# Kernel tuning notes

Measured on AMD Instinct MI355X. Metric: run time of the kernel, lower is better.

Reference implementation:

```python
import jax, jax.numpy as jnp
import numpy as np

NEG_INF = -2.0**32 + 1.0  # matches torch paddings value


def prelu(x, a):
    return jnp.where(x >= 0, x, a * x)


def setup_inputs() -> dict:
    key = jax.random.key(0)
    ks = jax.random.split(key, 12)
    B, L, D, A = 2048, 200, 128, 64
    return {
        "query": jax.random.normal(ks[0], (B, D), jnp.float32),
        "keys": jax.random.normal(ks[1], (B, L, D), jnp.float32),
        "keys_length": jax.random.randint(ks[2], (B,), 0, L, jnp.int64 if jax.config.jax_enable_x64 else jnp.int32),
        "W1": jax.random.normal(ks[3], (4 * D, A), jnp.float32) * (1.0 / np.sqrt(4 * D)),
        "b1": jax.random.normal(ks[4], (A,), jnp.float32) * 0.01,
        "a1": jnp.full((1,), 0.25, jnp.float32),  # PReLU default init
        "W2": jax.random.normal(ks[5], (A, A), jnp.float32) * (1.0 / np.sqrt(A)),
        "b2": jax.random.normal(ks[6], (A,), jnp.float32) * 0.01,
        "a2": jnp.full((1,), 0.25, jnp.float32),
        "W3": jax.random.normal(ks[7], (A, 1), jnp.float32) * (1.0 / np.sqrt(A)),
        "b3": jax.random.normal(ks[8], (1,), jnp.float32) * 0.01,
    }


def reference(query, keys, keys_length, W1, b1, a1, W2, b2, a2, W3, b3):
    B, L, D = keys.shape
    q = jnp.broadcast_to(query[:, None, :], (B, L, D))
    # concat features: [q, k, q-k, q*k] -> (B, L, 4D)
    q_k = jnp.concatenate([q, keys, q - keys, q * keys], axis=-1)
    h = prelu(jnp.einsum("blf,fa->bla", q_k, W1) + b1, a1)
    h = prelu(jnp.einsum("bla,ac->blc", h, W2) + b2, a2)
    scores = (jnp.einsum("bla,ao->blo", h, W3) + b3)[..., 0]  # (B, L)
    mask = jnp.arange(L)[None, :] < keys_length[:, None]
    scores = jnp.where(mask, scores, NEG_INF)
    att = jax.nn.softmax(scores, axis=1)
    out = jnp.einsum("bl,bld->bd", att, keys)  # bmm(att[:,None,:], keys)
    return out, att
```

## Files before the change

kernel.cpp:

```cpp
#include <hip/hip_runtime.h>
#include <math.h>

typedef __attribute__((ext_vector_type(8))) _Float16 half8;
typedef __attribute__((ext_vector_type(4))) float float4_t;

#define NB 2048
#define LL 200
#define DD 128
#define AA 64
#define NEG_INF_F -4294967295.0f

#define WQ_STRIDE 136
#define W2_STRIDE 72
#define H1_STRIDE 72

__global__ __launch_bounds__(256, 4)
void din_fused(const float* __restrict__ query,
               const float* __restrict__ keys,
               const int*   __restrict__ keys_length,
               const float* __restrict__ W1,
               const float* __restrict__ b1,
               const float* __restrict__ a1p,
               const float* __restrict__ W2,
               const float* __restrict__ b2,
               const float* __restrict__ a2p,
               const float* __restrict__ W3,
               float* __restrict__ out,
               float* __restrict__ att)
{
    __shared__ __align__(16) _Float16 sWqT[AA * WQ_STRIDE];
    __shared__ __align__(16) _Float16 sW2T[AA * W2_STRIDE];
    __shared__ __align__(16) _Float16 sH1[4 * 16 * H1_STRIDE];
    __shared__ float sQ[DD];
    __shared__ float sQW[AA];
    __shared__ float sS[224];
    __shared__ float sRed[256];

    const int tid  = threadIdx.x;
    const int b    = blockIdx.x;
    const int len  = keys_length[b];
    const float pa1 = a1p[0], pa2 = a2p[0];
    const int lane = tid & 63, wv = tid >> 6;
    const int col  = lane & 15, quad = lane >> 4;

    if (tid < DD) sQ[tid] = query[(size_t)b * DD + tid];
    for (int i = tid; i < 224; i += 256) sS[i] = NEG_INF_F;
    __syncthreads();

    for (int i = tid; i < DD * AA; i += 256) {
        const int d = i >> 6, a = i & 63;
        const float v = W1[(DD + d) * AA + a] - W1[(2 * DD + d) * AA + a]
                      + sQ[d] * W1[(3 * DD + d) * AA + a];
        sWqT[a * WQ_STRIDE + d] = (_Float16)v;
    }
    for (int i = tid; i < AA * AA; i += 256) {
        const int a = i >> 6, c = i & 63;
        sW2T[c * W2_STRIDE + a] = (_Float16)W2[i];
    }
    {
        const int a = tid & 63, p = tid >> 6;
        float acc = 0.f;
        for (int d = p * 32; d < p * 32 + 32; ++d)
            acc += sQ[d] * (W1[d * AA + a] + W1[(2 * DD + d) * AA + a]);
        sRed[tid] = acc;
    }
    __syncthreads();
    if (tid < AA)
        sQW[tid] = b1[tid] + sRed[tid] + sRed[64 + tid] + sRed[128 + tid] + sRed[192 + tid];
    __syncthreads();

    float qwreg[4], b2reg[4], w3reg[4];
    #pragma unroll
    for (int n = 0; n < 4; ++n) {
        qwreg[n] = sQW[n * 16 + col];
        b2reg[n] = b2[n * 16 + col];
        w3reg[n] = W3[n * 16 + col];
    }

    const int ntiles = (len + 15) >> 4;
    _Float16* const myH = &sH1[wv * 16 * H1_STRIDE];

    for (int t = wv; t < ntiles; t += 4) {
        const int l0 = t * 16;
        const int lrow = min(l0 + col, LL - 1);
        const float* const krow = keys + ((size_t)b * LL + lrow) * DD + quad * 8;

        float4_t C[4] = {{0,0,0,0},{0,0,0,0},{0,0,0,0},{0,0,0,0}};
        #pragma unroll
        for (int ks = 0; ks < 4; ++ks) {
            const float4 a0 = *(const float4*)(krow + ks * 32);
            const float4 a1 = *(const float4*)(krow + ks * 32 + 4);
            half8 af;
            af[0] = (_Float16)a0.x; af[1] = (_Float16)a0.y;
            af[2] = (_Float16)a0.z; af[3] = (_Float16)a0.w;
            af[4] = (_Float16)a1.x; af[5] = (_Float16)a1.y;
            af[6] = (_Float16)a1.z; af[7] = (_Float16)a1.w;
            const int ko = ks * 32 + quad * 8;
            #pragma unroll
            for (int n = 0; n < 4; ++n) {
                const half8 bf = *(const half8*)&sWqT[(n * 16 + col) * WQ_STRIDE + ko];
                C[n] = __builtin_amdgcn_mfma_f32_16x16x32_f16(af, bf, C[n], 0, 0, 0);
            }
        }
        #pragma unroll
        for (int n = 0; n < 4; ++n) {
            #pragma unroll
            for (int r = 0; r < 4; ++r) {
                float v = C[n][r] + qwreg[n];
                v = v >= 0.f ? v : pa1 * v;
                myH[(quad * 4 + r) * H1_STRIDE + n * 16 + col] = (_Float16)v;
            }
        }

        float4_t D[4] = {{0,0,0,0},{0,0,0,0},{0,0,0,0},{0,0,0,0}};
        #pragma unroll
        for (int ks = 0; ks < 2; ++ks) {
            const int ko = ks * 32 + quad * 8;
            const half8 af = *(const half8*)&myH[col * H1_STRIDE + ko];
            #pragma unroll
            for (int n = 0; n < 4; ++n) {
                const half8 bf = *(const half8*)&sW2T[(n * 16 + col) * W2_STRIDE + ko];
                D[n] = __builtin_amdgcn_mfma_f32_16x16x32_f16(af, bf, D[n], 0, 0, 0);
            }
        }
        float p[4] = {0.f, 0.f, 0.f, 0.f};
        #pragma unroll
        for (int n = 0; n < 4; ++n) {
            #pragma unroll
            for (int r = 0; r < 4; ++r) {
                float v = D[n][r] + b2reg[n];
                v = v >= 0.f ? v : pa2 * v;
                p[r] += v * w3reg[n];
            }
        }
        #pragma unroll
        for (int r = 0; r < 4; ++r) {
            float pv = p[r];
            pv += __shfl_xor(pv, 1);
            pv += __shfl_xor(pv, 2);
            pv += __shfl_xor(pv, 4);
            pv += __shfl_xor(pv, 8);
            const int l = l0 + quad * 4 + r;
            if (col == 0 && l < len) sS[l] = pv;
        }
    }

    __syncthreads();
    float m = (tid < LL) ? sS[tid] : -INFINITY;
    #pragma unroll
    for (int o = 1; o < 64; o <<= 1) m = fmaxf(m, __shfl_xor(m, o));
    if (lane == 0) sRed[wv] = m;
    __syncthreads();
    const float M = fmaxf(fmaxf(sRed[0], sRed[1]), fmaxf(sRed[2], sRed[3]));
    float e = (tid < LL) ? expf(sS[tid] - M) : 0.f;
    float s = e;
    #pragma unroll
    for (int o = 1; o < 64; o <<= 1) s += __shfl_xor(s, o);
    if (lane == 0) sRed[8 + wv] = s;
    __syncthreads();
    const float S = sRed[8] + sRed[9] + sRed[10] + sRed[11];
    const float inv = 1.f / S;
    if (tid < LL) {
        const float v = e * inv;
        sS[tid] = v;
        att[(size_t)b * LL + tid] = v;
    }
    __syncthreads();

    float2* const scratch = (float2*)sWqT;
    const int Lcap = (len == 0) ? LL : len;
    float2 a3 = make_float2(0.f, 0.f);
    const float* kb = keys + (size_t)b * LL * DD + (lane << 1);
    for (int l = wv; l < Lcap; l += 4) {
        const float w = sS[l];
        const float2 kv = *(const float2*)(kb + (size_t)l * DD);
        a3.x += w * kv.x; a3.y += w * kv.y;
    }
    scratch[tid] = a3;
    __syncthreads();
    if (tid < 64) {
        const float2 p0 = scratch[tid];
        const float2 p1 = scratch[64 + tid];
        const float2 p2 = scratch[128 + tid];
        const float2 p3 = scratch[192 + tid];
        float2 rr;
        rr.x = p0.x + p1.x + p2.x + p3.x;
        rr.y = p0.y + p1.y + p2.y + p3.y;
        *(float2*)(out + (size_t)b * DD + (lane << 1)) = rr;
    }
}

extern "C" void kernel_launch(void* const* d_in, const int* in_sizes, int n_in,
                              void* d_out, int out_size, void* d_ws, size_t ws_size,
                              hipStream_t stream) {
    (void)in_sizes; (void)n_in; (void)d_ws; (void)ws_size; (void)out_size;
    const float* query = (const float*)d_in[0];
    const float* keys  = (const float*)d_in[1];
    const int*   klen  = (const int*)d_in[2];
    const float* W1    = (const float*)d_in[3];
    const float* b1    = (const float*)d_in[4];
    const float* a1    = (const float*)d_in[5];
    const float* W2    = (const float*)d_in[6];
    const float* b2    = (const float*)d_in[7];
    const float* a2    = (const float*)d_in[8];
    const float* W3    = (const float*)d_in[9];

    float* out = (float*)d_out;
    float* att = out + (size_t)NB * DD;

    hipLaunchKernelGGL(din_fused, dim3(NB), dim3(256), 0, stream,
                       query, keys, klen, W1, b1, a1, W2, b2, a2, W3, out, att);
}
```

Measured before the change: 354.3 us.

## Split weight prep into separate kernel and batch two rows per block

Moves the per-batch folding of W1 into a prep kernel that builds a shared fp16 combined weight (k and q*k parts) plus per-batch query projection, so the main kernel no longer recomputes the 128x64 folded weight for every batch row. The main kernel now computes q*k on the fly as a second MFMA operand, doubling layer-1 MFMA work, and processes two batch rows per block with two waves each. W2 fragments are held in registers, and softmax is done per wave without cross-wave barriers. This adds a second launch and more register pressure, and it halves per-row parallelism over sequence tiles.

```diff
diff --git a/kernel.cpp b/kernel.cpp
--- a/kernel.cpp
+++ b/kernel.cpp
@@ -10,182 +10,252 @@
 #define AA 64
 #define NEG_INF_F -4294967295.0f
 
-#define WQ_STRIDE 136
-#define W2_STRIDE 72
+#define WC_STRIDE 264
 #define H1_STRIDE 72
 
-__global__ __launch_bounds__(256, 4)
-void din_fused(const float* __restrict__ query,
-               const float* __restrict__ keys,
-               const int*   __restrict__ keys_length,
-               const float* __restrict__ W1,
-               const float* __restrict__ b1,
-               const float* __restrict__ a1p,
-               const float* __restrict__ W2,
-               const float* __restrict__ b2,
-               const float* __restrict__ a2p,
-               const float* __restrict__ W3,
-               float* __restrict__ out,
-               float* __restrict__ att)
+#define WS_WC_BYTES   33792
+#define WS_W2T_OFF    33792
+#define WS_QA_OFF     43008
+
+__global__ __launch_bounds__(256)
+void din_prep(const float* __restrict__ query,
+              const float* __restrict__ W1,
+              const float* __restrict__ b1,
+              const float* __restrict__ W2,
+              _Float16* __restrict__ ws16,
+              float* __restrict__ qa)
 {
-    __shared__ __align__(16) _Float16 sWqT[AA * WQ_STRIDE];
-    __shared__ __align__(16) _Float16 sW2T[AA * W2_STRIDE];
+    const int tid = threadIdx.x;
+    const int blk = blockIdx.x;
+
+    if (blk < 128) {
+        __shared__ float sW1s[DD * AA];
+        __shared__ float sq[16 * DD];
+        const int b0 = blk * 16;
+        for (int i = tid; i < DD * AA; i += 256)
+            sW1s[i] = W1[i] + W1[2 * DD * AA + i];
+        for (int i = tid; i < 16 * DD; i += 256)
+            sq[i] = query[(size_t)b0 * DD + i];
+        __syncthreads();
+        const int lane = tid & 63, bb = tid >> 6;
+        for (int g = 0; g < 4; ++g) {
+            const int bi = bb * 4 + g;
+            float acc = b1[lane];
+            #pragma unroll 8
+            for (int d = 0; d < DD; ++d)
+                acc += sq[bi * DD + d] * sW1s[d * AA + lane];
+            qa[(size_t)(b0 + bi) * AA + lane] = acc;
+        }
+    } else if (blk == 128) {
+        const int a = tid >> 2, c = tid & 3, k0 = c * 64;
+        for (int kk = 0; kk < 8; ++kk) {
+            half8 v;
+            #pragma unroll
+            for (int j = 0; j < 8; ++j) {
+                const int k = k0 + kk * 8 + j;
+                float x;
+                if (k < DD) x = W1[(DD + k) * AA + a] - W1[(2 * DD + k) * AA + a];
+                else        x = W1[(2 * DD + k) * AA + a];
+                v[j] = (_Float16)x;
+            }
+            *(half8*)&ws16[a * WC_STRIDE + k0 + kk * 8] = v;
+        }
+    } else {
+        _Float16* w2t = ws16 + WS_W2T_OFF / 2;
+        const int c = tid >> 2, j0 = (tid & 3) * 16;
+        for (int ch = 0; ch < 2; ++ch) {
+            half8 v;
+            #pragma unroll
+            for (int j = 0; j < 8; ++j) {
+                const int a = j0 + ch * 8 + j;
+                v[j] = (_Float16)W2[a * AA + c];
+            }
+            *(half8*)&w2t[c * AA + j0 + ch * 8] = v;
+        }
+    }
+}
+
+__global__ __launch_bounds__(256, 3)
+void din_main(const float* __restrict__ keys,
+              const int*   __restrict__ keys_length,
+              const float* __restrict__ a1p,
+              const float* __restrict__ b2,
+              const float* __restrict__ a2p,
+              const float* __restrict__ W3,
+              const _Float16* __restrict__ ws16,
+              const float* __restrict__ qa,
+              const float* __restrict__ query,
+              float* __restrict__ out,
+              float* __restrict__ att)
+{
+    __shared__ __align__(16) _Float16 sWc[AA * WC_STRIDE];
     __shared__ __align__(16) _Float16 sH1[4 * 16 * H1_STRIDE];
-    __shared__ float sQ[DD];
-    __shared__ float sQW[AA];
-    __shared__ float sS[224];
-    __shared__ float sRed[256];
+    __shared__ float sS[2 * 224];
 
     const int tid  = threadIdx.x;
-    const int b    = blockIdx.x;
-    const int len  = keys_length[b];
-    const float pa1 = a1p[0], pa2 = a2p[0];
     const int lane = tid & 63, wv = tid >> 6;
     const int col  = lane & 15, quad = lane >> 4;
-
-    if (tid < DD) sQ[tid] = query[(size_t)b * DD + tid];
-    for (int i = tid; i < 224; i += 256) sS[i] = NEG_INF_F;
-    __syncthreads();
-
-    for (int i = tid; i < DD * AA; i += 256) {
-        const int d = i >> 6, a = i & 63;
-        const float v = W1[(DD + d) * AA + a] - W1[(2 * DD + d) * AA + a]
-                      + sQ[d] * W1[(3 * DD + d) * AA + a];
-        sWqT[a * WQ_STRIDE + d] = (_Float16)v;
-    }
-    for (int i = tid; i < AA * AA; i += 256) {
-        const int a = i >> 6, c = i & 63;
-        sW2T[c * W2_STRIDE + a] = (_Float16)W2[i];
-    }
-    {
-        const int a = tid & 63, p = tid >> 6;
-        float acc = 0.f;
-        for (int d = p * 32; d < p * 32 + 32; ++d)
-            acc += sQ[d] * (W1[d * AA + a] + W1[(2 * DD + d) * AA + a]);
-        sRed[tid] = acc;
-    }
-    __syncthreads();
-    if (tid < AA)
-        sQW[tid] = b1[tid] + sRed[tid] + sRed[64 + tid] + sRed[128 + tid] + sRed[192 + tid];
-    __syncthreads();
-
-    float qwreg[4], b2reg[4], w3reg[4];
+    const int p = wv >> 1, sub = wv & 1;
+    const int b = blockIdx.x * 2 + p;
+    const int len = keys_length[b];
+    const float pa1 = a1p[0], pa2 = a2p[0];
+
+    for (int i = tid; i < WS_WC_BYTES / 16; i += 256)
+        ((int4*)sWc)[i] = ((const int4*)ws16)[i];
+    for (int i = tid; i < 448; i += 256) sS[i] = NEG_INF_F;
+    __syncthreads();
+
+    const _Float16* w2t = ws16 + WS_W2T_OFF / 2;
+    half8 w2f[2][4];
+    #pragma unroll
+    for (int ks = 0; ks < 2; ++ks)
+        #pragma unroll
+        for (int n = 0; n < 4; ++n)
+            w2f[ks][n] = *(const half8*)&w2t[(n * 16 + col) * AA + ks * 32 + quad * 8];
+
+    float qareg[4], b2reg[4], w3reg[4];
     #pragma unroll
     for (int n = 0; n < 4; ++n) {
-        qwreg[n] = sQW[n * 16 + col];
+        qareg[n] = qa[(size_t)b * AA + n * 16 + col];
         b2reg[n] = b2[n * 16 + col];
         w3reg[n] = W3[n * 16 + col];
     }
+    float qf[4][8];
+    #pragma unroll
+    for (int ks = 0; ks < 4; ++ks) {
+        const float4 q0 = *(const float4*)(query + (size_t)b * DD + ks * 32 + quad * 8);
+        const float4 q1 = *(const float4*)(query + (size_t)b * DD + ks * 32 + quad * 8 + 4);
+        qf[ks][0] = q0.x; qf[ks][1] = q0.y; qf[ks][2] = q0.z; qf[ks][3] = q0.w;
+        qf[ks][4] = q1.x; qf[ks][5] = q1.y; qf[ks][6] = q1.z; qf[ks][7] = q1.w;
+    }
 
     const int ntiles = (len + 15) >> 4;
     _Float16* const myH = &sH1[wv * 16 * H1_STRIDE];
 
-    for (int t = wv; t < ntiles; t += 4) {
+    for (int t = sub; t < ntiles; t += 2) {
         const int l0 = t * 16;
-        const int lrow = min(l0 + col, LL - 1);
+        const int lrow = l0 + col < LL ? l0 + col : LL - 1;
         const float* const krow = keys + ((size_t)b * LL + lrow) * DD + quad * 8;
 
+        float4 kv[8];
+        #pragma unroll
+        for (int ks = 0; ks < 4; ++ks) {
+            kv[2 * ks]     = *(const float4*)(krow + ks * 32);
+            kv[2 * ks + 1] = *(const float4*)(krow + ks * 32 + 4);
+        }
+
         float4_t C[4] = {{0,0,0,0},{0,0,0,0},{0,0,0,0},{0,0,0,0}};
         #pragma unroll
         for (int ks = 0; ks < 4; ++ks) {
-            const float4 a0 = *(const float4*)(krow + ks * 32);
-            const float4 a1 = *(const float4*)(krow + ks * 32 + 4);
-            half8 af;
-            af[0] = (_Float16)a0.x; af[1] = (_Float16)a0.y;
-            af[2] = (_Float16)a0.z; af[3] = (_Float16)a0.w;
-            af[4] = (_Float16)a1.x; af[5] = (_Float16)a1.y;
-            af[6] = (_Float16)a1.z; af[7] = (_Float16)a1.w;
+            half8 afk, afq;
+            #pragma unroll
+            for (int j = 0; j < 4; ++j) {
+                const float ke0 = ((const float*)&kv[2 * ks])[j];
+                const float ke1 = ((const float*)&kv[2 * ks + 1])[j];
+                afk[j]     = (_Float16)ke0;
+                afk[4 + j] = (_Float16)ke1;
+                afq[j]     = (_Float16)(qf[ks][j] * ke0);
+                afq[4 + j] = (_Float16)(qf[ks][4 + j] * ke1);
+            }
             const int ko = ks * 32 + quad * 8;
             #pragma unroll
             for (int n = 0; n < 4; ++n) {
-                const half8 bf = *(const half8*)&sWqT[(n * 16 + col) * WQ_STRIDE + ko];
-                C[n] = __builtin_amdgcn_mfma_f32_16x16x32_f16(af, bf, C[n], 0, 0, 0);
-            }
-        }
-        #pragma unroll
-        for (int n = 0; n < 4; ++n) {
+                const half8 bfk = *(const half8*)&sWc[(n * 16 + col) * WC_STRIDE + ko];
+                C[n] = __builtin_amdgcn_mfma_f32_16x16x32_f16(afk, bfk, C[n], 0, 0, 0);
+            }
+            #pragma unroll
+            for (int n = 0; n < 4; ++n) {
+                const half8 bfq = *(const half8*)&sWc[(n * 16 + col) * WC_STRIDE + DD + ko];
+                C[n] = __builtin_amdgcn_mfma_f32_16x16x32_f16(afq, bfq, C[n], 0, 0, 0);
+            }
+        }
+        #pragma unroll
+        for (int n = 0; n < 4; ++n)
             #pragma unroll
             for (int r = 0; r < 4; ++r) {
-                float v = C[n][r] + qwreg[n];
+                float v = C[n][r] + qareg[n];
                 v = v >= 0.f ? v : pa1 * v;
                 myH[(quad * 4 + r) * H1_STRIDE + n * 16 + col] = (_Float16)v;
             }
-        }
 
         float4_t D[4] = {{0,0,0,0},{0,0,0,0},{0,0,0,0},{0,0,0,0}};
         #pragma unroll
         for (int ks = 0; ks < 2; ++ks) {
-            const int ko = ks * 32 + quad * 8;
-            const half8 af = *(const half8*)&myH[col * H1_STRIDE + ko];
-            #pragma unroll
-            for (int n = 0; n < 4; ++n) {
-                const half8 bf = *(const half8*)&sW2T[(n * 16 + col) * W2_STRIDE + ko];
-                D[n] = __builtin_amdgcn_mfma_f32_16x16x32_f16(af, bf, D[n], 0, 0, 0);
-            }
-        }
-        float p[4] = {0.f, 0.f, 0.f, 0.f};
-        #pragma unroll
-        for (int n = 0; n < 4; ++n) {
+            const half8 af = *(const half8*)&myH[col * H1_STRIDE + ks * 32 + quad * 8];
+            #pragma unroll
+            for (int n = 0; n < 4; ++n)
+                D[n] = __builtin_amdgcn_mfma_f32_16x16x32_f16(af, w2f[ks][n], D[n], 0, 0, 0);
+        }
+        float pr[4] = {0.f, 0.f, 0.f, 0.f};
+        #pragma unroll
+        for (int n = 0; n < 4; ++n)
             #pragma unroll
             for (int r = 0; r < 4; ++r) {
                 float v = D[n][r] + b2reg[n];
                 v = v >= 0.f ? v : pa2 * v;
-                p[r] += v * w3reg[n];
-            }
-        }
+                pr[r] += v * w3reg[n];
+            }
         #pragma unroll
         for (int r = 0; r < 4; ++r) {
-            float pv = p[r];
+            float pv = pr[r];
             pv += __shfl_xor(pv, 1);
             pv += __shfl_xor(pv, 2);
             pv += __shfl_xor(pv, 4);
             pv += __shfl_xor(pv, 8);
             const int l = l0 + quad * 4 + r;
-            if (col == 0 && l < len) sS[l] = pv;
-        }
-    }
-
-    __syncthreads();
-    float m = (tid < LL) ? sS[tid] : -INFINITY;
+            if (col == 0 && l < len) sS[p * 224 + l] = pv;
+        }
+    }
+
+    __syncthreads();
+
+    float sv[4];
+    #pragma unroll
+    for (int j = 0; j < 4; ++j) {
+        const int l = lane + 64 * j;
+        sv[j] = (l < LL) ? sS[p * 224 + l] : -INFINITY;
+    }
+    float m = fmaxf(fmaxf(sv[0], sv[1]), fmaxf(sv[2], sv[3]));
     #pragma unroll
     for (int o = 1; o < 64; o <<= 1) m = fmaxf(m, __shfl_xor(m, o));
-    if (lane == 0) sRed[wv] = m;
-    __syncthreads();
-    const float M = fmaxf(fmaxf(sRed[0], sRed[1]), fmaxf(sRed[2], sRed[3]));
-    float e = (tid < LL) ? expf(sS[tid] - M) : 0.f;
-    float s = e;
+    float e[4], s = 0.f;
+    #pragma unroll
+    for (int j = 0; j < 4; ++j) {
+        const int l = lane + 64 * j;
+        e[j] = (l < LL) ? expf(sv[j] - m) : 0.f;
+        s += e[j];
+    }
     #pragma unroll
     for (int o = 1; o < 64; o <<= 1) s += __shfl_xor(s, o);
-    if (lane == 0) sRed[8 + wv] = s;
-    __syncthreads();
-    const float S = sRed[8] + sRed[9] + sRed[10] + sRed[11];
-    const float inv = 1.f / S;
-    if (tid < LL) {
-        const float v = e * inv;
-        sS[tid] = v;
-        att[(size_t)b * LL + tid] = v;
-    }
-    __syncthreads();
-
-    float2* const scratch = (float2*)sWqT;
+    const float inv = 1.f / s;
+    if (sub == 0) {
+        #pragma unroll
+        for (int j = 0; j < 4; ++j) {
+            const int l = lane + 64 * j;
+            if (l < LL) {
+                const float v = e[j] * inv;
+                sS[p * 224 + l] = v;
+                att[(size_t)b * LL + l] = v;
+            }
+        }
+    }
+    __syncthreads();
+
     const int Lcap = (len == 0) ? LL : len;
-    float2 a3 = make_float2(0.f, 0.f);
+    float2 acc = make_float2(0.f, 0.f);
     const float* kb = keys + (size_t)b * LL * DD + (lane << 1);
-    for (int l = wv; l < Lcap; l += 4) {
-        const float w = sS[l];
-        const float2 kv = *(const float2*)(kb + (size_t)l * DD);
-        a3.x += w * kv.x; a3.y += w * kv.y;
-    }
-    scratch[tid] = a3;
-    __syncthreads();
-    if (tid < 64) {
-        const float2 p0 = scratch[tid];
-        const float2 p1 = scratch[64 + tid];
-        const float2 p2 = scratch[128 + tid];
-        const float2 p3 = scratch[192 + tid];
-        float2 rr;
-        rr.x = p0.x + p1.x + p2.x + p3.x;
-        rr.y = p0.y + p1.y + p2.y + p3.y;
+    for (int l = sub; l < Lcap; l += 2) {
+        const float w = sS[p * 224 + l];
+        const float2 kv2 = *(const float2*)(kb + (size_t)l * DD);
+        acc.x += w * kv2.x; acc.y += w * kv2.y;
+    }
+    float2* const sPS = (float2*)sH1;
+    sPS[wv * 64 + lane] = acc;
+    __syncthreads();
+    if (sub == 0) {
+        const float2 p0 = sPS[(2 * p) * 64 + lane];
+        const float2 p1 = sPS[(2 * p + 1) * 64 + lane];
+        float2 rr; rr.x = p0.x + p1.x; rr.y = p0.y + p1.y;
         *(float2*)(out + (size_t)b * DD + (lane << 1)) = rr;
     }
 }
@@ -193,7 +263,7 @@
 extern "C" void kernel_launch(void* const* d_in, const int* in_sizes, int n_in,
                               void* d_out, int out_size, void* d_ws, size_t ws_size,
                               hipStream_t stream) {
-    (void)in_sizes; (void)n_in; (void)d_ws; (void)ws_size; (void)out_size;
+    (void)in_sizes; (void)n_in; (void)ws_size; (void)out_size;
     const float* query = (const float*)d_in[0];
     const float* keys  = (const float*)d_in[1];
     const int*   klen  = (const int*)d_in[2];
@@ -205,9 +275,14 @@
     const float* a2    = (const float*)d_in[8];
     const float* W3    = (const float*)d_in[9];
 
+    _Float16* ws16 = (_Float16*)d_ws;
+    float*    qawk = (float*)((char*)d_ws + WS_QA_OFF);
+
     float* out = (float*)d_out;
     float* att = out + (size_t)NB * DD;
 
-    hipLaunchKernelGGL(din_fused, dim3(NB), dim3(256), 0, stream,
-                       query, keys, klen, W1, b1, a1, W2, b2, a2, W3, out, att);
+    hipLaunchKernelGGL(din_prep, dim3(130), dim3(256), 0, stream,
+                       query, W1, b1, W2, ws16, qawk);
+    hipLaunchKernelGGL(din_main, dim3(NB / 2), dim3(256), 0, stream,
+                       keys, klen, a1, b2, a2, W3, ws16, qawk, query, out, att);
 }
```

Result: slower. 504.7 us (+42.4%).
